# Optimization experiments

Hardware: AMD Instinct MI355X
Metric: run time of the kernel (lower is better)

The kernel has to match this reference:

```python
import jax, jax.numpy as jnp
import numpy as np

LOG_2PI = float(np.log(2.0 * np.pi))


def setup_inputs() -> dict:
    key = jax.random.key(0)
    ks = jax.random.split(key, 8)
    n_CBs, n_SBs = 8192, 4096
    nuc_locations = jax.random.normal(ks[0], (n_CBs, 2), dtype=jnp.float32)
    SB_locations = jax.random.normal(ks[1], (n_SBs, 2), dtype=jnp.float32)
    epsilon_perm = jax.random.uniform(ks[2], (n_CBs,), dtype=jnp.float32)
    epsilon = jax.random.uniform(ks[3], (n_CBs,), dtype=jnp.float32)
    d_drop = jax.random.uniform(ks[4], (n_CBs,), dtype=jnp.float32)
    rho_SB = jnp.ones((1,), dtype=jnp.float32)
    sigma_SB = jnp.ones((1,), dtype=jnp.float32)
    chi = jax.random.uniform(ks[5], (n_SBs,), dtype=jnp.float32)
    chi_ambient = chi / jnp.sum(chi)  # simplex constraint
    return {
        "nuc_locations": nuc_locations,
        "SB_locations": SB_locations,
        "epsilon_perm": epsilon_perm,
        "epsilon": epsilon,
        "d_drop": d_drop,
        "rho_SB": rho_SB,
        "sigma_SB": sigma_SB,
        "chi_ambient": chi_ambient,
    }


def _sb_concentrations(nuc, sb, epsilon_perm, rho_SB, sigma_SB):
    # Vectorized pairwise isotropic 2D Gaussian density.
    # MVN(loc=sb, cov=sigma*I_2).log_prob(nuc) = -log(2*pi) - log(sigma) - ||nuc-sb||^2/(2*sigma)
    sigma = sigma_SB[0]
    sq_n = jnp.sum(nuc * nuc, axis=-1)  # [N]
    sq_s = jnp.sum(sb * sb, axis=-1)    # [M]
    # squared distances via GEMM to avoid [N, M, 2] intermediate
    sq_dist = sq_n[:, None] + sq_s[None, :] - 2.0 * (nuc @ sb.T)  # [N, M]
    log_prob = -LOG_2PI - jnp.log(sigma) - sq_dist / (2.0 * sigma)
    return epsilon_perm[:, None] * rho_SB[0] * jnp.exp(log_prob)  # [N, M]


def reference(nuc_locations, SB_locations, epsilon_perm, epsilon, d_drop,
              rho_SB, sigma_SB, chi_ambient):
    k = _sb_concentrations(nuc_locations, SB_locations, epsilon_perm, rho_SB, sigma_SB)
    mu = epsilon[:, None] * k                                   # [N, M]
    lam = (epsilon * d_drop)[:, None] * chi_ambient[None, :]    # [N, M]
    return mu + lam  # Poisson rate for the observation model
```

## Files before the change

### kernel.cpp

```cpp
#include <hip/hip_runtime.h>


__global__ __launch_bounds__(256) void rate_kernel(
    const float* __restrict__ nuc,
    const float* __restrict__ sb,
    const float* __restrict__ epsilon_perm,
    const float* __restrict__ epsilon,
    const float* __restrict__ d_drop,
    const float* __restrict__ rho_SB,
    const float* __restrict__ sigma_SB,
    const float* __restrict__ chi,
    float* __restrict__ out,
    int M)
{
    const int row = blockIdx.x;
    const int tid = threadIdx.x;

    const float2 nxy = ((const float2*)nuc)[row];
    const float nx  = nxy.x;
    const float ny  = nxy.y;
    const float e   = epsilon[row];
    const float ep  = epsilon_perm[row];
    const float dd  = d_drop[row];
    const float rho = rho_SB[0];
    const float sig = sigma_SB[0];

    const float scale = (-0.5f / sig) * 1.4426950408889634f;
    const float coef = e * ep * rho * (0.15915494309189535f / sig);
    const float lamc = e * dd;

    float* orow = out + (size_t)row * (size_t)M;
    const float4* sb4  = (const float4*)sb;
    const float4* chi4 = (const float4*)chi;

    for (int j0 = tid * 4; j0 < M; j0 += 256 * 4) {
        const float4 s0 = sb4[j0 / 2];
        const float4 s1 = sb4[j0 / 2 + 1];
        const float4 cv = chi4[j0 / 4];

        const float sx[4] = { s0.x, s0.z, s1.x, s1.z };
        const float sy[4] = { s0.y, s0.w, s1.y, s1.w };
        const float ch[4] = { cv.x, cv.y, cv.z, cv.w };

        float4 res;
        float* resp = (float*)&res;
#pragma unroll
        for (int k = 0; k < 4; ++k) {
            const float dx = nx - sx[k];
            const float dy = ny - sy[k];
            const float d2 = fmaf(dx, dx, dy * dy);
            const float ev = exp2f(d2 * scale);
            resp[k] = fmaf(coef, ev, lamc * ch[k]);
        }
        *(float4*)(orow + j0) = res;
    }
}

extern "C" void kernel_launch(void* const* d_in, const int* in_sizes, int n_in,
                              void* d_out, int out_size, void* d_ws, size_t ws_size,
                              hipStream_t stream) {
    const float* nuc = (const float*)d_in[0];
    const float* sb  = (const float*)d_in[1];
    const float* epp = (const float*)d_in[2];
    const float* eps = (const float*)d_in[3];
    const float* ddp = (const float*)d_in[4];
    const float* rho = (const float*)d_in[5];
    const float* sig = (const float*)d_in[6];
    const float* chi = (const float*)d_in[7];
    float* out = (float*)d_out;

    const int M = in_sizes[7];
    const int N = out_size / M;

    rate_kernel<<<N, 256, 0, stream>>>(nuc, sb, epp, eps, ddp, rho, sig, chi, out, M);
}
```

Baseline: 175.0 us.

## Process four rows per block and use nontemporal stores for output

Each block now computes four output rows, so every sb/chi load is reused across four rows and the grid has a quarter as many blocks. Output writes use nontemporal vector stores to keep the large streaming output from polluting cache. A scalar tail kernel covers rows left over when N is not a multiple of four. The work is bound by the 128MB output write, so the gain depends mostly on store behaviour, and the fewer blocks could reduce overlap.

```diff
diff --git a/kernel.cpp b/kernel.cpp
--- a/kernel.cpp
+++ b/kernel.cpp
@@ -1,5 +1,9 @@
 #include <hip/hip_runtime.h>
 
+
+typedef float float4v __attribute__((ext_vector_type(4)));
+
+#define ROWS 4
 
 __global__ __launch_bounds__(256) void rate_kernel(
     const float* __restrict__ nuc,
@@ -13,23 +17,25 @@
     float* __restrict__ out,
     int M)
 {
-    const int row = blockIdx.x;
+    const int r0  = blockIdx.x * ROWS;
     const int tid = threadIdx.x;
 
-    const float2 nxy = ((const float2*)nuc)[row];
-    const float nx  = nxy.x;
-    const float ny  = nxy.y;
-    const float e   = epsilon[row];
-    const float ep  = epsilon_perm[row];
-    const float dd  = d_drop[row];
     const float rho = rho_SB[0];
     const float sig = sigma_SB[0];
+    const float scale = (-0.5f / sig) * 1.4426950408889634f;
+    const float cnorm = 0.15915494309189535f / sig;
 
-    const float scale = (-0.5f / sig) * 1.4426950408889634f;
-    const float coef = e * ep * rho * (0.15915494309189535f / sig);
-    const float lamc = e * dd;
+    float nx[ROWS], ny[ROWS], coef[ROWS], lamc[ROWS];
+#pragma unroll
+    for (int r = 0; r < ROWS; ++r) {
+        const float2 nxy = ((const float2*)nuc)[r0 + r];
+        nx[r] = nxy.x;
+        ny[r] = nxy.y;
+        const float e = epsilon[r0 + r];
+        coef[r] = e * epsilon_perm[r0 + r] * rho * cnorm;
+        lamc[r] = e * d_drop[r0 + r];
+    }
 
-    float* orow = out + (size_t)row * (size_t)M;
     const float4* sb4  = (const float4*)sb;
     const float4* chi4 = (const float4*)chi;
 
@@ -37,22 +43,48 @@
         const float4 s0 = sb4[j0 / 2];
         const float4 s1 = sb4[j0 / 2 + 1];
         const float4 cv = chi4[j0 / 4];
-
         const float sx[4] = { s0.x, s0.z, s1.x, s1.z };
         const float sy[4] = { s0.y, s0.w, s1.y, s1.w };
         const float ch[4] = { cv.x, cv.y, cv.z, cv.w };
 
-        float4 res;
-        float* resp = (float*)&res;
 #pragma unroll
-        for (int k = 0; k < 4; ++k) {
-            const float dx = nx - sx[k];
-            const float dy = ny - sy[k];
-            const float d2 = fmaf(dx, dx, dy * dy);
-            const float ev = exp2f(d2 * scale);
-            resp[k] = fmaf(coef, ev, lamc * ch[k]);
+        for (int r = 0; r < ROWS; ++r) {
+            float4v res;
+#pragma unroll
+            for (int k = 0; k < 4; ++k) {
+                const float dx = nx[r] - sx[k];
+                const float dy = ny[r] - sy[k];
+                const float d2 = fmaf(dx, dx, dy * dy);
+                const float ev = exp2f(d2 * scale);
+                res[k] = fmaf(coef[r], ev, lamc[r] * ch[k]);
+            }
+            __builtin_nontemporal_store(
+                res, (float4v*)(out + (size_t)(r0 + r) * (size_t)M + j0));
         }
-        *(float4*)(orow + j0) = res;
+    }
+}
+
+__global__ __launch_bounds__(256) void rate_kernel_1(
+    const float* __restrict__ nuc, const float* __restrict__ sb,
+    const float* __restrict__ epsilon_perm, const float* __restrict__ epsilon,
+    const float* __restrict__ d_drop, const float* __restrict__ rho_SB,
+    const float* __restrict__ sigma_SB, const float* __restrict__ chi,
+    float* __restrict__ out, int M, int row0)
+{
+    const int row = row0 + blockIdx.x;
+    const int tid = threadIdx.x;
+    const float2 nxy = ((const float2*)nuc)[row];
+    const float e   = epsilon[row];
+    const float sig = sigma_SB[0];
+    const float scale = (-0.5f / sig) * 1.4426950408889634f;
+    const float coef = e * epsilon_perm[row] * rho_SB[0] * (0.15915494309189535f / sig);
+    const float lamc = e * d_drop[row];
+    float* orow = out + (size_t)row * (size_t)M;
+    for (int j = tid; j < M; j += 256) {
+        const float dx = nxy.x - sb[2 * j];
+        const float dy = nxy.y - sb[2 * j + 1];
+        const float ev = exp2f(fmaf(dx, dx, dy * dy) * scale);
+        orow[j] = fmaf(coef, ev, lamc * chi[j]);
     }
 }
 
@@ -72,5 +104,12 @@
     const int M = in_sizes[7];
     const int N = out_size / M;
 
-    rate_kernel<<<N, 256, 0, stream>>>(nuc, sb, epp, eps, ddp, rho, sig, chi, out, M);
+    const int nb = N / ROWS;
+    if (nb > 0)
+        rate_kernel<<<nb, 256, 0, stream>>>(nuc, sb, epp, eps, ddp, rho, sig,
+                                            chi, out, M);
+    const int tail = N - nb * ROWS;
+    if (tail > 0)
+        rate_kernel_1<<<tail, 256, 0, stream>>>(nuc, sb, epp, eps, ddp, rho,
+                                                sig, chi, out, M, nb * ROWS);
 }
```

Measured after the change: 159.4 us. 8.9% less time.
